# Optimization experiments

Measured on AMD Instinct MI355X. Metric: run time of the kernel, lower is better.

## Reference

```python
import jax, jax.numpy as jnp
import numpy as np

N_USERS = 50000
N_ENT = 100000
N_INT = 5
EMB = 128
N_REL = 20
N_EDGES = 1000000
NNZ = 1000000
N_HOPS = 2
C_IDX = jnp.array([0, 1, 2, 3])
V_IDX = jnp.array([4, 5, 6, 7])
K_IDX = jnp.array([8, 9, 10, 11])
O_IDX = jnp.array([12, 13, 14, 15, 16, 17, 18, 19])


def setup_inputs() -> dict:
    key = jax.random.key(0)
    ks = jax.random.split(key, 9)
    return {
        "user_emb": jax.random.normal(ks[0], (N_USERS, EMB), jnp.float32) * 0.1,
        "entity_emb": jax.random.normal(ks[1], (N_ENT, EMB), jnp.float32) * 0.1,
        "intent_emb": jax.random.normal(ks[2], (N_INT, EMB), jnp.float32) * 0.1,
        "edge_index": jax.random.randint(ks[3], (2, N_EDGES), 0, N_ENT),
        "edge_type": jax.random.randint(ks[4], (N_EDGES,), 1, N_REL + 1),
        "interact_rows": jax.random.randint(ks[5], (NNZ,), 0, N_USERS),
        "interact_cols": jax.random.randint(ks[6], (NNZ,), 0, N_ENT),
        "interact_vals": jax.random.uniform(ks[7], (NNZ,), jnp.float32),
        "r_emb": jax.random.normal(ks[8], (N_REL, EMB), jnp.float32) * 0.1,
    }


def _scatter_mean(src, idx, n):
    s = jax.ops.segment_sum(src, idx, num_segments=n)
    c = jax.ops.segment_sum(jnp.ones((src.shape[0],), src.dtype), idx, num_segments=n)
    return jnp.where(c[:, None] > 0, s / jnp.maximum(c, 1.0)[:, None], 0.0)


def _intent_agg(vec, emb):
    # softmax over rows of (vec * emb).sum(-1), then attention-weighted mean
    att = jax.nn.softmax(jnp.sum(vec * emb, axis=1))
    return jnp.mean(att[:, None] * emb, axis=0)


def _l2norm(x):
    n = jnp.linalg.norm(x, axis=1, keepdims=True)
    return x / jnp.maximum(n, 1e-12)


def _dist_cor(t1, t2):
    d = t1.shape[0]
    t1 = t1[:, None]
    t2 = t2[:, None]
    a_ = 2.0 * (t1 @ t1.T)
    b_ = 2.0 * (t2 @ t2.T)
    t1s = t1 ** 2
    t2s = t2 ** 2
    a = jnp.sqrt(jnp.maximum(t1s - a_ + t1s.T, 0.0) + 1e-8)
    b = jnp.sqrt(jnp.maximum(t2s - b_ + t2s.T, 0.0) + 1e-8)
    A = a - a.mean(axis=0, keepdims=True) - a.mean(axis=1, keepdims=True) + a.mean()
    B = b - b.mean(axis=0, keepdims=True) - b.mean(axis=1, keepdims=True) + b.mean()
    d2 = float(d * d)
    dcov_AB = jnp.sqrt(jnp.maximum((A * B).sum() / d2, 0.0) + 1e-8)
    dcov_AA = jnp.sqrt(jnp.maximum((A * A).sum() / d2, 0.0) + 1e-8)
    dcov_BB = jnp.sqrt(jnp.maximum((B * B).sum() / d2, 0.0) + 1e-8)
    return dcov_AB / jnp.sqrt(dcov_AA * dcov_BB + 1e-8)


def _cul_cor(intent_emb):
    cor = 0.0
    for i in range(N_INT):
        for j in range(i + 1, N_INT):
            cor = cor + _dist_cor(intent_emb[i], intent_emb[j])
    return cor


def _forward(user_emb, entity_emb, intent_emb, edge_index, edge_type,
             interact_rows, interact_cols, interact_vals, r_emb):
    head, tail = edge_index[0], edge_index[1]
    cor = _cul_cor(intent_emb)
    res_e, res_u = entity_emb, user_emb
    e, u = entity_emb, user_emb
    for _ in range(N_HOPS):
        # edge gather-multiply-scatter_mean: [E,D]
        msg = e[tail] * r_emb[edge_type - 1]
        e_agg = _scatter_mean(msg, head, N_ENT)
        # intent attention over relation subsets
        all_intent = jnp.stack([
            _intent_agg(intent_emb[0], r_emb),
            _intent_agg(intent_emb[1], r_emb[C_IDX]),
            _intent_agg(intent_emb[2], r_emb[V_IDX]),
            _intent_agg(intent_emb[3], r_emb[K_IDX]),
            _intent_agg(intent_emb[4], r_emb[O_IDX]),
        ], axis=0)
        intent2 = (all_intent + intent_emb) / 2.0  # [5,D]
        # user-intent attention
        score = jax.nn.softmax(u @ intent2.T, axis=1)  # [U,5]
        # sparse.mm(interact_mat, entity_emb)
        u_agg = jax.ops.segment_sum(interact_vals[:, None] * e[interact_cols],
                                    interact_rows, num_segments=N_USERS)
        u_agg = u_agg * (score @ intent2) + u_agg
        e = _l2norm(e_agg)
        u = _l2norm(u_agg)
        res_e = res_e + e
        res_u = res_u + u
    return res_e, res_u, cor


def reference(user_emb, entity_emb, intent_emb, edge_index, edge_type,
              interact_rows, interact_cols, interact_vals, r_emb):
    return _forward(user_emb, entity_emb, intent_emb, edge_index, edge_type,
                    interact_rows, interact_cols, interact_vals, r_emb)
```

## Files before the change

kernel.cpp:

```cpp
#include <hip/hip_runtime.h>
#include <hip/hip_fp16.h>
#include <math.h>

#define N_USERS 50000
#define N_ENT   100000
#define N_INT   5
#define EMB     128
#define N_REL   20
#define N_EDGES 1000000
#define NNZ     1000000
#define SLOT    64
#define NPART   8
#define STAGE_CAP 131072
#define CSTRIDE 32
#define SITEMS  4
#define NCH     128
#define EBLOCKS (N_ENT/8)
#define UBLOCKS (N_USERS/8)

#define CORB    10
#define I2END   (CORB + N_INT)
#define CONVBLK 3125
#define CONVEND (I2END + CONVBLK)
#define STAGBLK 2048
#define MISCGRID (CONVEND + STAGBLK)

union F4H8 { float4 f4; __half2 h2[4]; };

__global__ __launch_bounds__(256) void misc_kernel(const float* __restrict__ intent,
                                                   const float* __restrict__ r_emb,
                                                   float* __restrict__ i2,
                                                   float* __restrict__ partial,
                                                   float* __restrict__ out_cor,
                                                   int* __restrict__ done,
                                                   const float2* __restrict__ conv_in,
                                                   __half2* __restrict__ conv_out,
                                                   const int* __restrict__ head,
                                                   const int* __restrict__ tail,
                                                   const int* __restrict__ etype,
                                                   const int* __restrict__ irows,
                                                   const int* __restrict__ icols,
                                                   const float* __restrict__ ivals,
                                                   int* __restrict__ cursor,
                                                   uint2* __restrict__ stage_e,
                                                   uint2* __restrict__ stage_u) {
    __shared__ float t1[EMB], t2[EMB], rma[EMB], rmb[EMB];
    __shared__ float red[256];
    __shared__ float sh_mean_a, sh_mean_b;
    __shared__ float dotsh[N_REL];
    __shared__ int l_cnt[2*NPART];
    __shared__ int l_base[2*NPART];
    const int tid = threadIdx.x;

    if (blockIdx.x < CORB) {
        const int p = blockIdx.x;
        const int pi[10] = {0,0,0,0,1,1,1,2,2,3};
        const int pj[10] = {1,2,3,4,2,3,4,3,4,4};

        if (tid < EMB) {
            t1[tid] = intent[pi[p]*EMB + tid];
            t2[tid] = intent[pj[p]*EMB + tid];
        }
        __syncthreads();
        if (tid < EMB) {
            float x1 = t1[tid], x2 = t2[tid];
            float sa = 0.f, sb = 0.f;
            for (int k = 0; k < EMB; ++k) {
                float da = x1 - t1[k];
                float db = x2 - t2[k];
                sa += sqrtf(da*da + 1e-8f);
                sb += sqrtf(db*db + 1e-8f);
            }
            rma[tid] = sa / (float)EMB;
            rmb[tid] = sb / (float)EMB;
        }
        __syncthreads();
        red[tid] = (tid < EMB) ? rma[tid] : 0.f;
        __syncthreads();
        for (int s = 128; s > 0; s >>= 1) { if (tid < s) red[tid] += red[tid+s]; __syncthreads(); }
        if (tid == 0) sh_mean_a = red[0] / (float)EMB;
        __syncthreads();
        red[tid] = (tid < EMB) ? rmb[tid] : 0.f;
        __syncthreads();
        for (int s = 128; s > 0; s >>= 1) { if (tid < s) red[tid] += red[tid+s]; __syncthreads(); }
        if (tid == 0) sh_mean_b = red[0] / (float)EMB;
        __syncthreads();
        const float mean_a = sh_mean_a, mean_b = sh_mean_b;

        float lab = 0.f, laa = 0.f, lbb = 0.f;
        for (int idx = tid; idx < EMB*EMB; idx += 256) {
            int r = idx >> 7, c = idx & (EMB-1);
            float da = t1[r] - t1[c];
            float db = t2[r] - t2[c];
            float av = sqrtf(da*da + 1e-8f);
            float bv = sqrtf(db*db + 1e-8f);
            float A = av - rma[r] - rma[c] + mean_a;
            float B = bv - rmb[r] - rmb[c] + mean_b;
            lab += A*B; laa += A*A; lbb += B*B;
        }
        red[tid] = lab; __syncthreads();
        for (int s = 128; s > 0; s >>= 1) { if (tid < s) red[tid] += red[tid+s]; __syncthreads(); }
        float sab = red[0]; __syncthreads();
        red[tid] = laa; __syncthreads();
        for (int s = 128; s > 0; s >>= 1) { if (tid < s) red[tid] += red[tid+s]; __syncthreads(); }
        float saa = red[0]; __syncthreads();
        red[tid] = lbb; __syncthreads();
        for (int s = 128; s > 0; s >>= 1) { if (tid < s) red[tid] += red[tid+s]; __syncthreads(); }
        float sbb = red[0]; __syncthreads();

        if (tid == 0) {
            const float d2 = (float)(EMB*EMB);
            float dab = sqrtf(fmaxf(sab/d2, 0.f) + 1e-8f);
            float daa = sqrtf(fmaxf(saa/d2, 0.f) + 1e-8f);
            float dbb = sqrtf(fmaxf(sbb/d2, 0.f) + 1e-8f);
            partial[p] = dab / sqrtf(daa*dbb + 1e-8f);
            __threadfence();
            int t = atomicAdd(done, 1);
            if (t == CORB - 1) {
                float s = 0.f;
                volatile float* vp = (volatile float*)partial;
                for (int i = 0; i < CORB; ++i) s += vp[i];
                out_cor[0] = s;
            }
        }
    } else if (blockIdx.x < I2END) {
        const int i = blockIdx.x - CORB;
        const int d = tid;
        int start, n;
        if      (i == 0) { start = 0;  n = 20; }
        else if (i == 1) { start = 0;  n = 4;  }
        else if (i == 2) { start = 4;  n = 4;  }
        else if (i == 3) { start = 8;  n = 4;  }
        else             { start = 12; n = 8;  }

        const float v = (d < EMB) ? intent[i*EMB + d] : 0.f;
        for (int j = 0; j < n; ++j) {
            if (d < EMB) red[d] = v * r_emb[(start+j)*EMB + d];
            __syncthreads();
            for (int s = 64; s > 0; s >>= 1) { if (d < s) red[d] += red[d+s]; __syncthreads(); }
            if (d == 0) dotsh[j] = red[0];
            __syncthreads();
        }
        if (d < EMB) {
            float m = -1e30f;
            for (int j = 0; j < n; ++j) m = fmaxf(m, dotsh[j]);
            float s = 0.f;
            float att[N_REL];
            for (int j = 0; j < n; ++j) { att[j] = expf(dotsh[j] - m); s += att[j]; }
            float out = 0.f;
            for (int j = 0; j < n; ++j) out += (att[j]/s) * r_emb[(start+j)*EMB + d];
            out /= (float)n;
            i2[i*EMB + d] = 0.5f * (out + v);
        }
    } else if (blockIdx.x < CONVEND) {
        const int base = (blockIdx.x - I2END) * 2048;
        #pragma unroll
        for (int t = 0; t < 8; ++t) {
            int idx = base + t*256 + tid;
            float2 v = conv_in[idx];
            conv_out[idx] = __floats2half2_rn(v.x, v.y);
        }
    } else {
        const int TOTAL = N_EDGES + NNZ;
        const int base = (blockIdx.x - CONVEND) * (256*SITEMS);

        if (tid < 2*NPART) l_cnt[tid] = 0;
        __syncthreads();

        int part[SITEMS], loc[SITEMS];
        unsigned w0[SITEMS], w1[SITEMS];
        bool act[SITEMS];
        #pragma unroll
        for (int t = 0; t < SITEMS; ++t) {
            const int i = base + t*256 + tid;
            act[t] = i < TOTAL;
            if (act[t]) {
                if (i < N_EDGES) {
                    int h = head[i];
                    part[t] = h / (N_ENT/NPART);
                    w0[t] = (unsigned)h;
                    w1[t] = (unsigned)(tail[i] | ((etype[i]-1) << 20));
                } else {
                    int j = i - N_EDGES;
                    int r = irows[j];
                    part[t] = NPART + r / (N_USERS/NPART);
                    unsigned q = (unsigned)(ivals[j]*32767.0f + 0.5f);
                    w0[t] = (unsigned)r;
                    w1[t] = (q << 17) | (unsigned)icols[j];
                }
                loc[t] = atomicAdd(&l_cnt[part[t]], 1);
            }
        }
        __syncthreads();
        if (tid < 2*NPART && l_cnt[tid] > 0)
            l_base[tid] = atomicAdd(&cursor[tid*CSTRIDE], l_cnt[tid]);
        __syncthreads();
        #pragma unroll
        for (int t = 0; t < SITEMS; ++t) {
            if (act[t]) {
                int pos = l_base[part[t]] + loc[t];
                if (pos < STAGE_CAP) {
                    if (part[t] < NPART)
                        stage_e[(size_t)part[t]*STAGE_CAP + pos] = make_uint2(w0[t], w1[t]);
                    else
                        stage_u[(size_t)(part[t]-NPART)*STAGE_CAP + pos] = make_uint2(w0[t], w1[t]);
                }
            }
        }
    }
}

__global__ __launch_bounds__(256) void scatter_kernel(const uint2* __restrict__ stage_e,
                                                      const uint2* __restrict__ stage_u,
                                                      const int* __restrict__ cursor,
                                                      int* __restrict__ cnt_e,
                                                      int* __restrict__ cnt_u,
                                                      int* __restrict__ sorted_e,
                                                      unsigned* __restrict__ sorted_u) {
    const int part = blockIdx.x & (NPART-1);
    const int cid  = blockIdx.x >> 3;
    const bool isE = cid < NCH;
    const int chunk = isE ? cid : cid - NCH;
    const int n = min(cursor[(isE ? part : NPART + part)*CSTRIDE], STAGE_CAP);
    const uint2* s = (isE ? stage_e : stage_u) + (size_t)part*STAGE_CAP;
    int* cnt = isE ? cnt_e : cnt_u;

    const int i0 = (chunk*256 + threadIdx.x) * 4;
    if (i0 >= n) return;
    const bool h1 = i0 + 1 < n, h2 = i0 + 2 < n, h3 = i0 + 3 < n;
    uint4 a = *(const uint4*)(s + i0);
    uint4 b;
    if (h2) b = *(const uint4*)(s + i0 + 2);
    int pos0 = atomicAdd(&cnt[a.x], 1);
    int pos1 = h1 ? atomicAdd(&cnt[a.z], 1) : 0;
    int pos2 = h2 ? atomicAdd(&cnt[b.x], 1) : 0;
    int pos3 = h3 ? atomicAdd(&cnt[b.z], 1) : 0;
    if (isE) {
        if (pos0 < SLOT)       sorted_e[(size_t)a.x*SLOT + pos0] = (int)a.y;
        if (h1 && pos1 < SLOT) sorted_e[(size_t)a.z*SLOT + pos1] = (int)a.w;
        if (h2 && pos2 < SLOT) sorted_e[(size_t)b.x*SLOT + pos2] = (int)b.y;
        if (h3 && pos3 < SLOT) sorted_e[(size_t)b.z*SLOT + pos3] = (int)b.w;
    } else {
        if (pos0 < SLOT)       sorted_u[(size_t)a.x*SLOT + pos0] = a.y;
        if (h1 && pos1 < SLOT) sorted_u[(size_t)a.z*SLOT + pos1] = a.w;
        if (h2 && pos2 < SLOT) sorted_u[(size_t)b.x*SLOT + pos2] = b.y;
        if (h3 && pos3 < SLOT) sorted_u[(size_t)b.z*SLOT + pos3] = b.w;
    }
}

__global__ __launch_bounds__(256) void gather_eu_kernel(const __half2* __restrict__ e_tab,
                                                        const int* __restrict__ cnt_e,
                                                        const int* __restrict__ sorted_e,
                                                        const float* __restrict__ r_emb,
                                                        const float2* __restrict__ base_e,
                                                        float2* __restrict__ res_e,
                                                        __half2* __restrict__ e_out,
                                                        const int* __restrict__ cnt_u,
                                                        const unsigned* __restrict__ sorted_u,
                                                        const float2* __restrict__ u_prev,
                                                        const float* __restrict__ i2,
                                                        const float2* __restrict__ base_u,
                                                        float2* __restrict__ res_u,
                                                        float2* __restrict__ u_out,
                                                        int store, int write_res) {
    __shared__ float2 s_i2[N_INT*64];
    __shared__ float  tr[4][2][132];

    const int wv   = threadIdx.x >> 6;
    const int lane = threadIdx.x & 63;
    const int g = lane >> 4, sl = lane & 15;
    const float4* e4 = (const float4*)e_tab;

    if (blockIdx.x < EBLOCKS) {
        const int row0 = blockIdx.x*8 + wv*2;
        const int row1 = row0 + 1;
        const int deg0 = min(cnt_e[row0], SLOT);
        const int deg1 = min(cnt_e[row1], SLOT);
        int p0 = (lane < deg0) ? sorted_e[(size_t)row0*SLOT + lane] : 0;
        int p1 = (lane < deg1) ? sorted_e[(size_t)row1*SLOT + lane] : 0;

        const float4* r4 = (const float4*)r_emb;
        float accA[8] = {0,0,0,0,0,0,0,0};
        float accB[8] = {0,0,0,0,0,0,0,0};

#define EFMA(ACC, RAW, PM) do { \
            F4H8 u_; u_.f4 = (RAW); \
            const __half* h_ = (const __half*)u_.h2; \
            const int rr_ = (PM) >> 20; \
            float4 w0_ = r4[rr_*32 + sl*2]; \
            float4 w1_ = r4[rr_*32 + sl*2 + 1]; \
            ACC[0] += __half2float(h_[0]) * w0_.x; \
            ACC[1] += __half2float(h_[1]) * w0_.y; \
            ACC[2] += __half2float(h_[2]) * w0_.z; \
            ACC[3] += __half2float(h_[3]) * w0_.w; \
            ACC[4] += __half2float(h_[4]) * w1_.x; \
            ACC[5] += __half2float(h_[5]) * w1_.y; \
            ACC[6] += __half2float(h_[6]) * w1_.z; \
            ACC[7] += __half2float(h_[7]) * w1_.w; \
        } while (0)

        const int dm = max(deg0, deg1);
        for (int k = 0; k < dm; k += 8) {
            const int meA = k + g, meB = k + 4 + g;
            const int pm00 = __shfl(p0, meA), pm01 = __shfl(p0, meB);
            const int pm10 = __shfl(p1, meA), pm11 = __shfl(p1, meB);
            const bool a00 = meA < deg0, a01 = meB < deg0;
            const bool a10 = meA < deg1, a11 = meB < deg1;
            float4 r00, r01, r10, r11;
            if (a00) r00 = e4[(size_t)(pm00 & 0xFFFFF)*16 + sl];
            if (a01) r01 = e4[(size_t)(pm01 & 0xFFFFF)*16 + sl];
            if (a10) r10 = e4[(size_t)(pm10 & 0xFFFFF)*16 + sl];
            if (a11) r11 = e4[(size_t)(pm11 & 0xFFFFF)*16 + sl];
            if (a00) EFMA(accA, r00, pm00);
            if (a01) EFMA(accA, r01, pm01);
            if (a10) EFMA(accB, r10, pm10);
            if (a11) EFMA(accB, r11, pm11);
        }
#undef EFMA

        #pragma unroll
        for (int j = 0; j < 8; ++j) {
            accA[j] += __shfl_xor(accA[j], 16);
            accA[j] += __shfl_xor(accA[j], 32);
            accB[j] += __shfl_xor(accB[j], 16);
            accB[j] += __shfl_xor(accB[j], 32);
        }
        const float invA = (deg0 > 0) ? 1.0f/(float)deg0 : 0.0f;
        const float invB = (deg1 > 0) ? 1.0f/(float)deg1 : 0.0f;
        float ssA = 0.f, ssB = 0.f;
        #pragma unroll
        for (int j = 0; j < 8; ++j) {
            accA[j] *= invA; ssA += accA[j]*accA[j];
            accB[j] *= invB; ssB += accB[j]*accB[j];
        }
        #pragma unroll
        for (int o = 8; o > 0; o >>= 1) {
            ssA += __shfl_xor(ssA, o);
            ssB += __shfl_xor(ssB, o);
        }
        const float invnA = 1.0f / fmaxf(sqrtf(ssA), 1e-12f);
        const float invnB = 1.0f / fmaxf(sqrtf(ssB), 1e-12f);
        #pragma unroll
        for (int j = 0; j < 8; ++j) { accA[j] *= invnA; accB[j] *= invnB; }

#define EPI(ROW, ACC) do { \
            size_t r16 = (size_t)(ROW)*16 + sl; \
            if (store) { \
                F4H8 u_; \
                u_.h2[0] = __floats2half2_rn(ACC[0], ACC[1]); \
                u_.h2[1] = __floats2half2_rn(ACC[2], ACC[3]); \
                u_.h2[2] = __floats2half2_rn(ACC[4], ACC[5]); \
                u_.h2[3] = __floats2half2_rn(ACC[6], ACC[7]); \
                ((float4*)e_out)[r16] = u_.f4; \
            } \
            if (write_res) { \
                F4H8 pv; pv.f4 = ((const float4*)e_tab)[r16]; \
                const float4* b4 = (const float4*)base_e; \
                float4 ba = b4[(size_t)(ROW)*32 + sl*2]; \
                float4 bb = b4[(size_t)(ROW)*32 + sl*2 + 1]; \
                float2 q0 = __half22float2(pv.h2[0]); \
                float2 q1 = __half22float2(pv.h2[1]); \
                float2 q2 = __half22float2(pv.h2[2]); \
                float2 q3 = __half22float2(pv.h2[3]); \
                float4 ra = make_float4(ba.x + q0.x + ACC[0], ba.y + q0.y + ACC[1], \
                                        ba.z + q1.x + ACC[2], ba.w + q1.y + ACC[3]); \
                float4 rb = make_float4(bb.x + q2.x + ACC[4], bb.y + q2.y + ACC[5], \
                                        bb.z + q3.x + ACC[6], bb.w + q3.y + ACC[7]); \
                ((float4*)res_e)[(size_t)(ROW)*32 + sl*2]     = ra; \
                ((float4*)res_e)[(size_t)(ROW)*32 + sl*2 + 1] = rb; \
            } \
        } while (0)

        if (g == 0)      EPI(row0, accA);
        else if (g == 1) EPI(row1, accB);
#undef EPI
    } else {
        for (int k = threadIdx.x; k < N_INT*64; k += 256) s_i2[k] = ((const float2*)i2)[k];
        __syncthreads();
        const int ub = blockIdx.x - EBLOCKS;
        const int row0 = ub*8 + wv*2;
        const int row1 = row0 + 1;
        const int deg0 = min(cnt_u[row0], SLOT);
        const int deg1 = min(cnt_u[row1], SLOT);
        unsigned p0 = (lane < deg0) ? sorted_u[(size_t)row0*SLOT + lane] : 0u;
        unsigned p1 = (lane < deg1) ? sorted_u[(size_t)row1*SLOT + lane] : 0u;

        const float qs = 1.0f/32767.0f;
        float accA[8] = {0,0,0,0,0,0,0,0};
        float accB[8] = {0,0,0,0,0,0,0,0};

#define UFMA(ACC, RAW, Q) do { \
            F4H8 u_; u_.f4 = (RAW); \
            const __half* h_ = (const __half*)u_.h2; \
            const float v_ = (float)((Q) >> 17) * qs; \
            ACC[0] += v_ * __half2float(h_[0]); \
            ACC[1] += v_ * __half2float(h_[1]); \
            ACC[2] += v_ * __half2float(h_[2]); \
            ACC[3] += v_ * __half2float(h_[3]); \
            ACC[4] += v_ * __half2float(h_[4]); \
            ACC[5] += v_ * __half2float(h_[5]); \
            ACC[6] += v_ * __half2float(h_[6]); \
            ACC[7] += v_ * __half2float(h_[7]); \
        } while (0)

        const int dm = max(deg0, deg1);
        for (int k = 0; k < dm; k += 8) {
            const int meA = k + g, meB = k + 4 + g;
            const unsigned q00 = __shfl(p0, meA), q01 = __shfl(p0, meB);
            const unsigned q10 = __shfl(p1, meA), q11 = __shfl(p1, meB);
            const bool a00 = meA < deg0, a01 = meB < deg0;
            const bool a10 = meA < deg1, a11 = meB < deg1;
            float4 r00, r01, r10, r11;
            if (a00) r00 = e4[(size_t)(q00 & 0x1FFFFu)*16 + sl];
            if (a01) r01 = e4[(size_t)(q01 & 0x1FFFFu)*16 + sl];
            if (a10) r10 = e4[(size_t)(q10 & 0x1FFFFu)*16 + sl];
            if (a11) r11 = e4[(size_t)(q11 & 0x1FFFFu)*16 + sl];
            if (a00) UFMA(accA, r00, q00);
            if (a01) UFMA(accA, r01, q01);
            if (a10) UFMA(accB, r10, q10);
            if (a11) UFMA(accB, r11, q11);
        }
#undef UFMA

        #pragma unroll
        for (int j = 0; j < 8; ++j) {
            accA[j] += __shfl_xor(accA[j], 16);
            accA[j] += __shfl_xor(accA[j], 32);
            accB[j] += __shfl_xor(accB[j], 16);
            accB[j] += __shfl_xor(accB[j], 32);
        }
        if (g == 0) {
            #pragma unroll
            for (int j = 0; j < 8; ++j) tr[wv][0][sl*8 + j] = accA[j];
        } else if (g == 1) {
            #pragma unroll
            for (int j = 0; j < 8; ++j) tr[wv][1][sl*8 + j] = accB[j];
        }
        __syncthreads();
        const float s00 = tr[wv][0][2*lane], s01 = tr[wv][0][2*lane + 1];
        const float s10 = tr[wv][1][2*lane], s11 = tr[wv][1][2*lane + 1];

        const size_t o0 = (size_t)row0*64 + lane;
        const size_t o1 = (size_t)row1*64 + lane;
        const float2 up0 = u_prev[o0];
        const float2 up1 = u_prev[o1];
        float dot0[N_INT], dot1[N_INT];
        #pragma unroll
        for (int i = 0; i < N_INT; ++i) {
            float2 w = s_i2[i*64 + lane];
            float pr0 = up0.x*w.x + up0.y*w.y;
            float pr1 = up1.x*w.x + up1.y*w.y;
            #pragma unroll
            for (int o = 32; o > 0; o >>= 1) {
                pr0 += __shfl_xor(pr0, o);
                pr1 += __shfl_xor(pr1, o);
            }
            dot0[i] = pr0; dot1[i] = pr1;
        }
        float m0 = dot0[0], m1 = dot1[0];
        #pragma unroll
        for (int i = 1; i < N_INT; ++i) { m0 = fmaxf(m0, dot0[i]); m1 = fmaxf(m1, dot1[i]); }
        float sm0 = 0.f, sm1 = 0.f;
        #pragma unroll
        for (int i = 0; i < N_INT; ++i) {
            dot0[i] = expf(dot0[i] - m0); sm0 += dot0[i];
            dot1[i] = expf(dot1[i] - m1); sm1 += dot1[i];
        }
        float f00 = 0.f, f01 = 0.f, f10 = 0.f, f11 = 0.f;
        #pragma unroll
        for (int i = 0; i < N_INT; ++i) {
            float a0 = dot0[i] / sm0;
            float a1 = dot1[i] / sm1;
            float2 w = s_i2[i*64 + lane];
            f00 += a0*w.x; f01 += a0*w.y;
            f10 += a1*w.x; f11 += a1*w.y;
        }
        float x00 = s00 * (1.0f + f00), x01 = s01 * (1.0f + f01);
        float x10 = s10 * (1.0f + f10), x11 = s11 * (1.0f + f11);
        float ss0 = x00*x00 + x01*x01;
        float ss1 = x10*x10 + x11*x11;
        #pragma unroll
        for (int o = 32; o > 0; o >>= 1) {
            ss0 += __shfl_xor(ss0, o);
            ss1 += __shfl_xor(ss1, o);
        }
        const float invn0 = 1.0f / fmaxf(sqrtf(ss0), 1e-12f);
        const float invn1 = 1.0f / fmaxf(sqrtf(ss1), 1e-12f);
        x00 *= invn0; x01 *= invn0;
        x10 *= invn1; x11 *= invn1;
        if (store) {
            u_out[o0] = make_float2(x00, x01);
            u_out[o1] = make_float2(x10, x11);
        }
        if (write_res) {
            float2 b0 = base_u[o0];
            float2 b1 = base_u[o1];
            res_u[o0] = make_float2(b0.x + up0.x + x00, b0.y + up0.y + x01);
            res_u[o1] = make_float2(b1.x + up1.x + x10, b1.y + up1.y + x11);
        }
    }
}

extern "C" void kernel_launch(void* const* d_in, const int* in_sizes, int n_in,
                              void* d_out, int out_size, void* d_ws, size_t ws_size,
                              hipStream_t stream) {
    const float* user_emb   = (const float*)d_in[0];
    const float* entity_emb = (const float*)d_in[1];
    const float* intent_emb = (const float*)d_in[2];
    const int*   edge_index = (const int*)  d_in[3];
    const int*   edge_type  = (const int*)  d_in[4];
    const int*   irows      = (const int*)  d_in[5];
    const int*   icols      = (const int*)  d_in[6];
    const float* ivals      = (const float*)d_in[7];
    const float* r_emb      = (const float*)d_in[8];

    float* out     = (float*)d_out;
    float* res_e   = out;
    float* res_u   = out + (size_t)N_ENT*EMB;
    float* out_cor = out + (size_t)N_ENT*EMB + (size_t)N_USERS*EMB;

    const int* head = edge_index;
    const int* tail = edge_index + N_EDGES;

    char* ws = (char*)d_ws;
    __half2* entF16 = (__half2*)ws;  ws += (size_t)N_ENT*EMB*2;
    __half2* eA     = (__half2*)ws;  ws += (size_t)N_ENT*EMB*2;
    float2*  uA     = (float2*)ws;   ws += (size_t)N_USERS*EMB*4;
    int*     sorted_e = (int*)ws;    ws += (size_t)N_ENT*SLOT*4;
    unsigned* sorted_u = (unsigned*)ws; ws += (size_t)N_USERS*SLOT*4;
    char* zbase = ws;
    int* cnt_e = (int*)ws;           ws += (size_t)N_ENT*4;
    int* cnt_u = (int*)ws;           ws += (size_t)N_USERS*4;
    int* cursor = (int*)ws;          ws += 2*NPART*CSTRIDE*4;
    int* done   = (int*)ws;          ws += 128;
    size_t zbytes = (size_t)(ws - zbase);
    float* i2  = (float*)ws;         ws += N_INT*EMB*4;
    float* ws_cor = (float*)ws;      ws += 16*4;

    uint2* stage_e = (uint2*)eA;
    uint2* stage_u = (uint2*)uA;

    hipMemsetAsync(zbase, 0, zbytes, stream);

    misc_kernel<<<MISCGRID, 256, 0, stream>>>(intent_emb, r_emb, i2,
                                              ws_cor, out_cor, done,
                                              (const float2*)entity_emb, entF16,
                                              head, tail, edge_type,
                                              irows, icols, ivals,
                                              cursor, stage_e, stage_u);

    scatter_kernel<<<NPART*2*NCH, 256, 0, stream>>>(stage_e, stage_u, cursor,
                                                    cnt_e, cnt_u, sorted_e, sorted_u);

    const float2* ent2 = (const float2*)entity_emb;
    const float2* usr2 = (const float2*)user_emb;

    gather_eu_kernel<<<EBLOCKS + UBLOCKS, 256, 0, stream>>>(
        entF16, cnt_e, sorted_e, r_emb, ent2, (float2*)res_e, eA,
        cnt_u, sorted_u, usr2, i2, usr2, (float2*)res_u, uA, 1, 0);

    gather_eu_kernel<<<EBLOCKS + UBLOCKS, 256, 0, stream>>>(
        eA, cnt_e, sorted_e, r_emb, ent2, (float2*)res_e, eA,
        cnt_u, sorted_u, (const float2*)uA, i2, usr2, (float2*)res_u, uA, 0, 1);
}
```

Measured before the change: 449.8 us.

## Replace two-pass partitioned staging with direct atomic bucketing in misc kernel

Drops the partition-staging pass and the separate scatter kernel. Edges and interactions are now bucketed straight into the per-row slot arrays with global atomics inside misc_kernel, and the build blocks are placed before the fp16 conversion blocks. This removes one kernel launch and the write and re-read of 16 MB of staging data. The cost is atomics and scattered writes spread over the whole count and slot arrays instead of partition-local regions, which could hurt cache locality.

Measured after the change: 439.5 us. 1.02x faster.

```diff
diff --git a/kernel.cpp b/kernel.cpp
--- a/kernel.cpp
+++ b/kernel.cpp
@@ -10,20 +10,16 @@
 #define N_EDGES 1000000
 #define NNZ     1000000
 #define SLOT    64
-#define NPART   8
-#define STAGE_CAP 131072
-#define CSTRIDE 32
 #define SITEMS  4
-#define NCH     128
 #define EBLOCKS (N_ENT/8)
 #define UBLOCKS (N_USERS/8)
 
 #define CORB    10
 #define I2END   (CORB + N_INT)
+#define BLDBLK  2048
+#define BLDEND  (I2END + BLDBLK)
 #define CONVBLK 3125
-#define CONVEND (I2END + CONVBLK)
-#define STAGBLK 2048
-#define MISCGRID (CONVEND + STAGBLK)
+#define MISCGRID (BLDEND + CONVBLK)
 
 union F4H8 { float4 f4; __half2 h2[4]; };
 
@@ -41,15 +37,14 @@
                                                    const int* __restrict__ irows,
                                                    const int* __restrict__ icols,
                                                    const float* __restrict__ ivals,
-                                                   int* __restrict__ cursor,
-                                                   uint2* __restrict__ stage_e,
-                                                   uint2* __restrict__ stage_u) {
+                                                   int* __restrict__ cnt_e,
+                                                   int* __restrict__ cnt_u,
+                                                   int* __restrict__ sorted_e,
+                                                   unsigned* __restrict__ sorted_u) {
     __shared__ float t1[EMB], t2[EMB], rma[EMB], rmb[EMB];
     __shared__ float red[256];
     __shared__ float sh_mean_a, sh_mean_b;
     __shared__ float dotsh[N_REL];
-    __shared__ int l_cnt[2*NPART];
-    __shared__ int l_base[2*NPART];
     const int tid = threadIdx.x;
 
     if (blockIdx.x < CORB) {
@@ -152,99 +147,48 @@
             out /= (float)n;
             i2[i*EMB + d] = 0.5f * (out + v);
         }
-    } else if (blockIdx.x < CONVEND) {
-        const int base = (blockIdx.x - I2END) * 2048;
+    } else if (blockIdx.x < BLDEND) {
+        const int TOTAL = N_EDGES + NNZ;
+        const int base = (blockIdx.x - I2END) * (256*SITEMS);
+
+        int rows[SITEMS]; unsigned words[SITEMS];
+        bool act[SITEMS], isE[SITEMS];
+        #pragma unroll
+        for (int t = 0; t < SITEMS; ++t) {
+            const int i = base + t*256 + tid;
+            act[t] = i < TOTAL;
+            isE[t] = i < N_EDGES;
+            if (act[t]) {
+                if (isE[t]) {
+                    rows[t]  = head[i];
+                    words[t] = (unsigned)(tail[i] | ((etype[i]-1) << 20));
+                } else {
+                    int j = i - N_EDGES;
+                    rows[t]  = irows[j];
+                    unsigned q = (unsigned)(ivals[j]*32767.0f + 0.5f);
+                    words[t] = (q << 17) | (unsigned)icols[j];
+                }
+            }
+        }
+        int pos[SITEMS];
+        #pragma unroll
+        for (int t = 0; t < SITEMS; ++t)
+            if (act[t]) pos[t] = atomicAdd(isE[t] ? &cnt_e[rows[t]] : &cnt_u[rows[t]], 1);
+        #pragma unroll
+        for (int t = 0; t < SITEMS; ++t) {
+            if (act[t] && pos[t] < SLOT) {
+                if (isE[t]) sorted_e[(size_t)rows[t]*SLOT + pos[t]] = (int)words[t];
+                else        sorted_u[(size_t)rows[t]*SLOT + pos[t]] = words[t];
+            }
+        }
+    } else {
+        const int base = (blockIdx.x - BLDEND) * 2048;
         #pragma unroll
         for (int t = 0; t < 8; ++t) {
             int idx = base + t*256 + tid;
             float2 v = conv_in[idx];
             conv_out[idx] = __floats2half2_rn(v.x, v.y);
         }
-    } else {
-        const int TOTAL = N_EDGES + NNZ;
-        const int base = (blockIdx.x - CONVEND) * (256*SITEMS);
-
-        if (tid < 2*NPART) l_cnt[tid] = 0;
-        __syncthreads();
-
-        int part[SITEMS], loc[SITEMS];
-        unsigned w0[SITEMS], w1[SITEMS];
-        bool act[SITEMS];
-        #pragma unroll
-        for (int t = 0; t < SITEMS; ++t) {
-            const int i = base + t*256 + tid;
-            act[t] = i < TOTAL;
-            if (act[t]) {
-                if (i < N_EDGES) {
-                    int h = head[i];
-                    part[t] = h / (N_ENT/NPART);
-                    w0[t] = (unsigned)h;
-                    w1[t] = (unsigned)(tail[i] | ((etype[i]-1) << 20));
-                } else {
-                    int j = i - N_EDGES;
-                    int r = irows[j];
-                    part[t] = NPART + r / (N_USERS/NPART);
-                    unsigned q = (unsigned)(ivals[j]*32767.0f + 0.5f);
-                    w0[t] = (unsigned)r;
-                    w1[t] = (q << 17) | (unsigned)icols[j];
-                }
-                loc[t] = atomicAdd(&l_cnt[part[t]], 1);
-            }
-        }
-        __syncthreads();
-        if (tid < 2*NPART && l_cnt[tid] > 0)
-            l_base[tid] = atomicAdd(&cursor[tid*CSTRIDE], l_cnt[tid]);
-        __syncthreads();
-        #pragma unroll
-        for (int t = 0; t < SITEMS; ++t) {
-            if (act[t]) {
-                int pos = l_base[part[t]] + loc[t];
-                if (pos < STAGE_CAP) {
-                    if (part[t] < NPART)
-                        stage_e[(size_t)part[t]*STAGE_CAP + pos] = make_uint2(w0[t], w1[t]);
-                    else
-                        stage_u[(size_t)(part[t]-NPART)*STAGE_CAP + pos] = make_uint2(w0[t], w1[t]);
-                }
-            }
-        }
-    }
-}
-
-__global__ __launch_bounds__(256) void scatter_kernel(const uint2* __restrict__ stage_e,
-                                                      const uint2* __restrict__ stage_u,
-                                                      const int* __restrict__ cursor,
-                                                      int* __restrict__ cnt_e,
-                                                      int* __restrict__ cnt_u,
-                                                      int* __restrict__ sorted_e,
-                                                      unsigned* __restrict__ sorted_u) {
-    const int part = blockIdx.x & (NPART-1);
-    const int cid  = blockIdx.x >> 3;
-    const bool isE = cid < NCH;
-    const int chunk = isE ? cid : cid - NCH;
-    const int n = min(cursor[(isE ? part : NPART + part)*CSTRIDE], STAGE_CAP);
-    const uint2* s = (isE ? stage_e : stage_u) + (size_t)part*STAGE_CAP;
-    int* cnt = isE ? cnt_e : cnt_u;
-
-    const int i0 = (chunk*256 + threadIdx.x) * 4;
-    if (i0 >= n) return;
-    const bool h1 = i0 + 1 < n, h2 = i0 + 2 < n, h3 = i0 + 3 < n;
-    uint4 a = *(const uint4*)(s + i0);
-    uint4 b;
-    if (h2) b = *(const uint4*)(s + i0 + 2);
-    int pos0 = atomicAdd(&cnt[a.x], 1);
-    int pos1 = h1 ? atomicAdd(&cnt[a.z], 1) : 0;
-    int pos2 = h2 ? atomicAdd(&cnt[b.x], 1) : 0;
-    int pos3 = h3 ? atomicAdd(&cnt[b.z], 1) : 0;
-    if (isE) {
-        if (pos0 < SLOT)       sorted_e[(size_t)a.x*SLOT + pos0] = (int)a.y;
-        if (h1 && pos1 < SLOT) sorted_e[(size_t)a.z*SLOT + pos1] = (int)a.w;
-        if (h2 && pos2 < SLOT) sorted_e[(size_t)b.x*SLOT + pos2] = (int)b.y;
-        if (h3 && pos3 < SLOT) sorted_e[(size_t)b.z*SLOT + pos3] = (int)b.w;
-    } else {
-        if (pos0 < SLOT)       sorted_u[(size_t)a.x*SLOT + pos0] = a.y;
-        if (h1 && pos1 < SLOT) sorted_u[(size_t)a.z*SLOT + pos1] = a.w;
-        if (h2 && pos2 < SLOT) sorted_u[(size_t)b.x*SLOT + pos2] = b.y;
-        if (h3 && pos3 < SLOT) sorted_u[(size_t)b.z*SLOT + pos3] = b.w;
     }
 }
 
@@ -531,14 +475,10 @@
     char* zbase = ws;
     int* cnt_e = (int*)ws;           ws += (size_t)N_ENT*4;
     int* cnt_u = (int*)ws;           ws += (size_t)N_USERS*4;
-    int* cursor = (int*)ws;          ws += 2*NPART*CSTRIDE*4;
     int* done   = (int*)ws;          ws += 128;
     size_t zbytes = (size_t)(ws - zbase);
     float* i2  = (float*)ws;         ws += N_INT*EMB*4;
     float* ws_cor = (float*)ws;      ws += 16*4;
-
-    uint2* stage_e = (uint2*)eA;
-    uint2* stage_u = (uint2*)uA;
 
     hipMemsetAsync(zbase, 0, zbytes, stream);
 
@@ -547,10 +487,7 @@
                                               (const float2*)entity_emb, entF16,
                                               head, tail, edge_type,
                                               irows, icols, ivals,
-                                              cursor, stage_e, stage_u);
-
-    scatter_kernel<<<NPART*2*NCH, 256, 0, stream>>>(stage_e, stage_u, cursor,
-                                                    cnt_e, cnt_u, sorted_e, sorted_u);
+                                              cnt_e, cnt_u, sorted_e, sorted_u);
 
     const float2* ent2 = (const float2*)entity_emb;
     const float2* usr2 = (const float2*)user_emb;
```
